# Kernel tuning notes

Hardware: AMD Instinct MI355X
Metric: run time of the kernel (lower is better)

Reference implementation:

```python
import jax, jax.numpy as jnp
import numpy as np

B, T, V, H, NH, NLVL = 64, 2048, 256, 64, 4, 2
HD = H // NH  # 16
EPS = 1e-5


def setup_inputs() -> dict:
    key = jax.random.key(0)
    ks = jax.random.split(key, 16)
    s = 0.05
    return {
        "x": jax.random.randint(ks[0], (B, T), 0, V),
        "emb": jax.random.normal(ks[1], (V, H), dtype=jnp.float32) * s,
        # LSTM params, PyTorch gate order i, f, g, o stacked along dim 0
        "w_ih": jax.random.normal(ks[2], (4 * H, H), dtype=jnp.float32) * s,
        "w_hh": jax.random.normal(ks[3], (4 * H, H), dtype=jnp.float32) * s,
        "b_ih": jax.random.normal(ks[4], (4 * H,), dtype=jnp.float32) * s,
        "b_hh": jax.random.normal(ks[5], (4 * H,), dtype=jnp.float32) * s,
        # two MHA levels, packed qkv in_proj like nn.MultiheadAttention
        "wqkv": jax.random.normal(ks[6], (NLVL, 3 * H, H), dtype=jnp.float32) * s,
        "bqkv": jax.random.normal(ks[7], (NLVL, 3 * H), dtype=jnp.float32) * s,
        "wo": jax.random.normal(ks[8], (NLVL, H, H), dtype=jnp.float32) * s,
        "bo": jax.random.normal(ks[9], (NLVL, H), dtype=jnp.float32) * s,
        "ln_g": jnp.ones((H,), dtype=jnp.float32),
        "ln_b": jnp.zeros((H,), dtype=jnp.float32),
        "fc_w": jax.random.normal(ks[10], (V, H), dtype=jnp.float32) * s,
        "fc_b": jax.random.normal(ks[11], (V,), dtype=jnp.float32) * s,
    }


def _lstm(x, w_ih, w_hh, b_ih, b_hh):
    # x: (B, T, H) -> (B, T, H); single layer, PyTorch gate order i,f,g,o
    b = x.shape[0]
    h0 = jnp.zeros((b, H), x.dtype)
    c0 = jnp.zeros((b, H), x.dtype)

    def step(carry, xt):
        h, c = carry
        g = xt @ w_ih.T + b_ih + h @ w_hh.T + b_hh  # (B, 4H)
        i, f, gg, o = jnp.split(g, 4, axis=-1)
        c = jax.nn.sigmoid(f) * c + jax.nn.sigmoid(i) * jnp.tanh(gg)
        h = jax.nn.sigmoid(o) * jnpp_tanh(c) if False else jax.nn.sigmoid(o) * jnp.tanh(c)
        return (h, c), h

    _, hs = jax.lax.scan(step, (h0, c0), jnp.swapaxes(x, 0, 1))  # (T, B, H)
    return jnp.swapaxes(hs, 0, 1)


def _mha(x, wqkv, bqkv, wo, bo):
    # Faithful to nn.MultiheadAttention with batch_first=False:
    # x: (L, N, E) where here L = batch dim of lstm_out, N = seq dim.
    L, N, E = x.shape
    qkv = x @ wqkv.T + bqkv  # (L, N, 3E)
    q, k, v = jnp.split(qkv, 3, axis=-1)
    q = q.reshape(L, N, NH, HD)
    k = k.reshape(L, N, NH, HD)
    v = v.reshape(L, N, NH, HD)
    scale = jnp.asarray(1.0 / np.sqrt(HD), x.dtype)
    att = jax.nn.softmax(jnp.einsum('lnhd,mnhd->nhlm', q, k) * scale, axis=-1)
    o = jnp.einsum('nhlm,mnhd->lnhd', att, v).reshape(L, N, E)
    return o @ wo.T + bo


def reference(x, emb, w_ih, w_hh, b_ih, b_hh, wqkv, bqkv, wo, bo, ln_g, ln_b, fc_w, fc_b):
    h = emb[x]  # (B, T, H)
    h = _lstm(h, w_ih, w_hh, b_ih, b_hh)  # (B, T, H)
    for l in range(NLVL):
        h = _mha(h, wqkv[l], bqkv[l], wo[l], bo[l])
    mu = jnp.mean(h, axis=-1, keepdims=True)
    var = jnp.mean(jnp.square(h - mu), axis=-1, keepdims=True)  # biased, like torch LN
    hn = (h - mu) * jax.lax.rsqrt(var + EPS) * ln_g + ln_b
    return hn @ fc_w.T + fc_b  # (B, T, V)
```

## Files before the change

### kernel.cpp

```cpp
#include <hip/hip_runtime.h>

enum { TT = 2048, HH = 64, BB = 64, GG = 256, VV = 256 };

static __device__ __forceinline__ void bar_lds(){
  asm volatile("s_waitcnt lgkmcnt(0)\n\ts_barrier" ::: "memory");
}

__global__ __launch_bounds__(256) void k_embw(const float* __restrict__ emb,
                                              const float* __restrict__ w_ih,
                                              const float* __restrict__ b_ih,
                                              const float* __restrict__ b_hh,
                                              float* __restrict__ embW){
  int v = blockIdx.x, g = threadIdx.x;
  __shared__ float e[HH];
  if (g < HH) e[g] = emb[v*HH + g];
  bar_lds();
  float acc = b_ih[g] + b_hh[g];
  const float* wr = w_ih + g*HH;
#pragma unroll
  for (int k = 0; k < HH; k += 4){
    float4 w4 = *(const float4*)(wr + k);
    acc = fmaf(e[k],   w4.x, acc); acc = fmaf(e[k+1], w4.y, acc);
    acc = fmaf(e[k+2], w4.z, acc); acc = fmaf(e[k+3], w4.w, acc);
  }
  embW[v*GG + g] = acc;
}

__global__ __launch_bounds__(256) void k_lstm(const int* __restrict__ x,
                                              const float* __restrict__ embW,
                                              const float* __restrict__ w_hh,
                                              float* __restrict__ hout){
  int b = blockIdx.x, g = threadIdx.x;
  __shared__ float hsh[HH];
  __shared__ float gsh[GG];
  float w[HH];
  {
    const float* wr = w_hh + g*HH;
#pragma unroll
    for (int k = 0; k < HH; k += 4)
      *(float4*)&w[k] = *(const float4*)(wr + k);
  }
  if (g < HH) hsh[g] = 0.f;
  float c = 0.f;
  const int* xb = x + b*TT;
  int i0 = xb[0];
  float gx = embW[i0*GG + g];
  int i1 = xb[1];
  const bool istanh = ((g >> 6) == 2);
  float* houtb = hout + (size_t)b*TT*HH;
  bar_lds();
#pragma unroll 2
  for (int t = 0; t < TT; t++){
    float gxn = embW[i1*GG + g];
    int inx = xb[(t + 2 < TT) ? (t + 2) : (TT - 1)];
    float a0 = 0.f, a1 = 0.f, a2 = 0.f, a3 = 0.f;
#pragma unroll
    for (int k = 0; k < 16; k += 4){
      float4 h0 = *(const float4*)&hsh[k];
      float4 h1 = *(const float4*)&hsh[16 + k];
      float4 h2 = *(const float4*)&hsh[32 + k];
      float4 h3 = *(const float4*)&hsh[48 + k];
      a0 = fmaf(w[k],      h0.x, a0); a0 = fmaf(w[k+1],    h0.y, a0);
      a0 = fmaf(w[k+2],    h0.z, a0); a0 = fmaf(w[k+3],    h0.w, a0);
      a1 = fmaf(w[16+k],   h1.x, a1); a1 = fmaf(w[16+k+1], h1.y, a1);
      a1 = fmaf(w[16+k+2], h1.z, a1); a1 = fmaf(w[16+k+3], h1.w, a1);
      a2 = fmaf(w[32+k],   h2.x, a2); a2 = fmaf(w[32+k+1], h2.y, a2);
      a2 = fmaf(w[32+k+2], h2.z, a2); a2 = fmaf(w[32+k+3], h2.w, a2);
      a3 = fmaf(w[48+k],   h3.x, a3); a3 = fmaf(w[48+k+1], h3.y, a3);
      a3 = fmaf(w[48+k+2], h3.z, a3); a3 = fmaf(w[48+k+3], h3.w, a3);
    }
    float acc = ((a0 + a1) + (a2 + a3)) + gx;
    float val;
    if (istanh) val = 1.f - 2.f/(__expf(2.f*acc) + 1.f);
    else        val = 1.f/(1.f + __expf(-acc));
    gsh[g] = val;
    bar_lds();
    if (g < HH){
      float i_ = gsh[g], f_ = gsh[HH+g], gg = gsh[128+g], o_ = gsh[192+g];
      c = fmaf(f_, c, i_*gg);
      float th = 1.f - 2.f/(__expf(2.f*c) + 1.f);
      float hv = o_*th;
      hsh[g] = hv;
      houtb[(size_t)t*HH + g] = hv;
    }
    bar_lds();
    gx = gxn; i1 = inx;
  }
}

__global__ __launch_bounds__(256) void k_mha(const float* __restrict__ hin,
                                             const float* __restrict__ wqkv,
                                             const float* __restrict__ bqkv,
                                             const float* __restrict__ wo,
                                             const float* __restrict__ bo,
                                             float* __restrict__ hout){
  int t = blockIdx.x, tid = threadIdx.x;
  __shared__ float xta[BB][HH];
  __shared__ float qkvs[BB][192];

  float wq[HH]; float bq = 0.f;
  if (tid < 192){
#pragma unroll
    for (int k = 0; k < HH; k += 4)
      *(float4*)&wq[k] = *(const float4*)(wqkv + tid*HH + k);
    bq = bqkv[tid];
  }
  {
    int r = tid >> 2, q = tid & 3;
    const float* p = hin + (size_t)(r*TT + t)*HH + q*16;
#pragma unroll
    for (int j = 0; j < 16; j += 4)
      *(float4*)&xta[r][q*16 + j] = *(const float4*)(p + j);
  }
  bar_lds();
  if (tid < 192){
#pragma unroll 4
    for (int b = 0; b < BB; b++){
      float acc = bq;
#pragma unroll
      for (int k = 0; k < HH; k += 4){
        float4 xv = *(const float4*)&xta[b][k];
        acc = fmaf(wq[k],   xv.x, acc); acc = fmaf(wq[k+1], xv.y, acc);
        acc = fmaf(wq[k+2], xv.z, acc); acc = fmaf(wq[k+3], xv.w, acc);
      }
      qkvs[b][tid] = acc;
    }
  }
  bar_lds();
  {
    int hd = tid >> 6, l = tid & 63;
    int qo = hd*16, ko = 64 + hd*16, vo = 128 + hd*16;
    float4 q0 = *(const float4*)&qkvs[l][qo];
    float4 q1 = *(const float4*)&qkvs[l][qo+4];
    float4 q2 = *(const float4*)&qkvs[l][qo+8];
    float4 q3 = *(const float4*)&qkvs[l][qo+12];
    float S[BB];
#pragma unroll
    for (int m = 0; m < BB; m++){
      float4 k0 = *(const float4*)&qkvs[m][ko];
      float4 k1 = *(const float4*)&qkvs[m][ko+4];
      float4 k2 = *(const float4*)&qkvs[m][ko+8];
      float4 k3 = *(const float4*)&qkvs[m][ko+12];
      float d;
      d = q0.x*k0.x;         d = fmaf(q0.y,k0.y,d); d = fmaf(q0.z,k0.z,d); d = fmaf(q0.w,k0.w,d);
      d = fmaf(q1.x,k1.x,d); d = fmaf(q1.y,k1.y,d); d = fmaf(q1.z,k1.z,d); d = fmaf(q1.w,k1.w,d);
      d = fmaf(q2.x,k2.x,d); d = fmaf(q2.y,k2.y,d); d = fmaf(q2.z,k2.z,d); d = fmaf(q2.w,k2.w,d);
      d = fmaf(q3.x,k3.x,d); d = fmaf(q3.y,k3.y,d); d = fmaf(q3.z,k3.z,d); d = fmaf(q3.w,k3.w,d);
      S[m] = 0.25f*d;
    }
    float mx = S[0];
#pragma unroll
    for (int m = 1; m < BB; m++) mx = fmaxf(mx, S[m]);
    float sum = 0.f;
#pragma unroll
    for (int m = 0; m < BB; m++){ S[m] = __expf(S[m] - mx); sum += S[m]; }
    float inv = 1.f/sum;
    float4 a0 = make_float4(0,0,0,0), a1 = a0, a2 = a0, a3 = a0;
#pragma unroll
    for (int m = 0; m < BB; m++){
      float s = S[m];
      float4 v0 = *(const float4*)&qkvs[m][vo];
      float4 v1 = *(const float4*)&qkvs[m][vo+4];
      float4 v2 = *(const float4*)&qkvs[m][vo+8];
      float4 v3 = *(const float4*)&qkvs[m][vo+12];
      a0.x = fmaf(s,v0.x,a0.x); a0.y = fmaf(s,v0.y,a0.y); a0.z = fmaf(s,v0.z,a0.z); a0.w = fmaf(s,v0.w,a0.w);
      a1.x = fmaf(s,v1.x,a1.x); a1.y = fmaf(s,v1.y,a1.y); a1.z = fmaf(s,v1.z,a1.z); a1.w = fmaf(s,v1.w,a1.w);
      a2.x = fmaf(s,v2.x,a2.x); a2.y = fmaf(s,v2.y,a2.y); a2.z = fmaf(s,v2.z,a2.z); a2.w = fmaf(s,v2.w,a2.w);
      a3.x = fmaf(s,v3.x,a3.x); a3.y = fmaf(s,v3.y,a3.y); a3.z = fmaf(s,v3.z,a3.z); a3.w = fmaf(s,v3.w,a3.w);
    }
    a0.x*=inv; a0.y*=inv; a0.z*=inv; a0.w*=inv;
    a1.x*=inv; a1.y*=inv; a1.z*=inv; a1.w*=inv;
    a2.x*=inv; a2.y*=inv; a2.z*=inv; a2.w*=inv;
    a3.x*=inv; a3.y*=inv; a3.z*=inv; a3.w*=inv;
    bar_lds();
    *(float4*)&xta[l][qo]    = a0;
    *(float4*)&xta[l][qo+4]  = a1;
    *(float4*)&xta[l][qo+8]  = a2;
    *(float4*)&xta[l][qo+12] = a3;
  }
  bar_lds();
  {
    int c = tid & 63, wg = tid >> 6;
    float wor[HH];
#pragma unroll
    for (int k = 0; k < HH; k += 4)
      *(float4*)&wor[k] = *(const float4*)(wo + c*HH + k);
    float bo4 = bo[c];
#pragma unroll 2
    for (int j = 0; j < 16; j++){
      int b = wg*16 + j;
      float acc = bo4;
#pragma unroll
      for (int k = 0; k < HH; k += 4){
        float4 xv = *(const float4*)&xta[b][k];
        acc = fmaf(wor[k],   xv.x, acc); acc = fmaf(wor[k+1], xv.y, acc);
        acc = fmaf(wor[k+2], xv.z, acc); acc = fmaf(wor[k+3], xv.w, acc);
      }
      hout[(size_t)(b*TT + t)*HH + c] = acc;
    }
  }
}

__global__ __launch_bounds__(256) void k_fc(const float* __restrict__ hin,
                                            const float* __restrict__ ln_g,
                                            const float* __restrict__ ln_b,
                                            const float* __restrict__ fc_w,
                                            const float* __restrict__ fc_b,
                                            float* __restrict__ out){
  int tid = threadIdx.x;
  __shared__ float tile[64][68];
  __shared__ float ps[64][4];
  __shared__ float pq[64][4];
  __shared__ float mu[64], rs[64];
  float w[HH];
  float wsum = 0.f, bias2 = fc_b[tid];
#pragma unroll
  for (int k = 0; k < HH; k += 4){
    float4 wv = *(const float4*)(fc_w + tid*HH + k);
    float4 gv = *(const float4*)(ln_g + k);
    float4 bv = *(const float4*)(ln_b + k);
    bias2 = fmaf(bv.x, wv.x, bias2); bias2 = fmaf(bv.y, wv.y, bias2);
    bias2 = fmaf(bv.z, wv.z, bias2); bias2 = fmaf(bv.w, wv.w, bias2);
    w[k]   = gv.x*wv.x; w[k+1] = gv.y*wv.y;
    w[k+2] = gv.z*wv.z; w[k+3] = gv.w*wv.w;
    wsum += w[k] + w[k+1] + w[k+2] + w[k+3];
  }
  int r = tid >> 2, q = tid & 3;
  for (int ti = 0; ti < 4; ti++){
    int rowbase = blockIdx.x*256 + ti*64;
    const float* p = hin + (size_t)(rowbase + r)*HH + q*16;
    float xv[16];
#pragma unroll
    for (int j = 0; j < 16; j += 4)
      *(float4*)&xv[j] = *(const float4*)(p + j);
    float s1 = 0.f, s2 = 0.f;
#pragma unroll
    for (int j = 0; j < 16; j++){ s1 += xv[j]; s2 = fmaf(xv[j], xv[j], s2); }
#pragma unroll
    for (int j = 0; j < 16; j += 4)
      *(float4*)&tile[r][q*16 + j] = *(const float4*)&xv[j];
    ps[r][q] = s1; pq[r][q] = s2;
    bar_lds();
    if (tid < 64){
      float4 a  = *(const float4*)&ps[tid][0];
      float4 b4 = *(const float4*)&pq[tid][0];
      float m = (a.x + a.y + a.z + a.w) * (1.f/64.f);
      float v = (b4.x + b4.y + b4.z + b4.w) * (1.f/64.f) - m*m;
      mu[tid] = m;
      rs[tid] = rsqrtf(v + 1e-5f);
    }
    bar_lds();
#pragma unroll 2
    for (int rr = 0; rr < 64; rr++){
      float acc = 0.f;
#pragma unroll
      for (int k = 0; k < HH; k += 4){
        float4 x4 = *(const float4*)&tile[rr][k];
        acc = fmaf(w[k],   x4.x, acc); acc = fmaf(w[k+1], x4.y, acc);
        acc = fmaf(w[k+2], x4.z, acc); acc = fmaf(w[k+3], x4.w, acc);
      }
      float o = rs[rr]*(acc - mu[rr]*wsum) + bias2;
      out[(size_t)(rowbase + rr)*VV + tid] = o;
    }
    bar_lds();
  }
}

extern "C" void kernel_launch(void* const* d_in, const int* in_sizes, int n_in,
                              void* d_out, int out_size, void* d_ws, size_t ws_size,
                              hipStream_t stream){
  (void)in_sizes; (void)n_in; (void)out_size; (void)ws_size;
  const int*   x    = (const int*)d_in[0];
  const float* emb  = (const float*)d_in[1];
  const float* w_ih = (const float*)d_in[2];
  const float* w_hh = (const float*)d_in[3];
  const float* b_ih = (const float*)d_in[4];
  const float* b_hh = (const float*)d_in[5];
  const float* wqkv = (const float*)d_in[6];
  const float* bqkv = (const float*)d_in[7];
  const float* wo   = (const float*)d_in[8];
  const float* bo   = (const float*)d_in[9];
  const float* ln_g = (const float*)d_in[10];
  const float* ln_b = (const float*)d_in[11];
  const float* fc_w = (const float*)d_in[12];
  const float* fc_b = (const float*)d_in[13];

  char* ws = (char*)d_ws;
  float* embW = (float*)ws;
  float* bufA = (float*)(ws + (1<<20));
  float* bufB = bufA + (size_t)BB*TT*HH;

  k_embw<<<VV,  256, 0, stream>>>(emb, w_ih, b_ih, b_hh, embW);
  k_lstm<<<BB,  256, 0, stream>>>(x, embW, w_hh, bufA);
  k_mha <<<TT,  256, 0, stream>>>(bufA, wqkv,          bqkv,       wo,          bo,      bufB);
  k_mha <<<TT,  256, 0, stream>>>(bufB, wqkv + 192*64, bqkv + 192, wo + 64*64,  bo + 64, bufA);
  k_fc  <<<512, 256, 0, stream>>>(bufA, ln_g, ln_b, fc_w, fc_b, (float*)d_out);
}
```

Before: 1.760 ms.

## Exchange LSTM gates via wave shuffles and double-buffer hidden state

Threads are remapped so that each wavefront holds the i, f, g and o gate rows for the same 16 hidden elements. Gate values are then combined with cross-lane shuffles instead of being written to and read back from shared memory. The hidden state is double-buffered in LDS, which removes one of the two block barriers in every one of the 2048 serial timesteps. The tanh gate is rewritten as a scaled sigmoid so all lanes take the same branch-free path. In exchange, three quarters of the lanes compute a cell update that is thrown away.

```diff
diff --git a/kernel.cpp b/kernel.cpp
--- a/kernel.cpp
+++ b/kernel.cpp
@@ -30,36 +30,40 @@
                                               const float* __restrict__ embW,
                                               const float* __restrict__ w_hh,
                                               float* __restrict__ hout){
-  int b = blockIdx.x, g = threadIdx.x;
-  __shared__ float hsh[HH];
-  __shared__ float gsh[GG];
+  int b = blockIdx.x, tid = threadIdx.x;
+  int wq = tid >> 6, l = tid & 63;
+  int grp = l >> 4, sub = l & 15;
+  int elem = wq*16 + sub;
+  int row  = grp*64 + elem;
+  __shared__ __align__(16) float hbuf[2][HH];
   float w[HH];
   {
-    const float* wr = w_hh + g*HH;
+    const float* wr = w_hh + row*HH;
 #pragma unroll
     for (int k = 0; k < HH; k += 4)
       *(float4*)&w[k] = *(const float4*)(wr + k);
   }
-  if (g < HH) hsh[g] = 0.f;
+  if (tid < HH) hbuf[0][tid] = 0.f;
   float c = 0.f;
   const int* xb = x + b*TT;
   int i0 = xb[0];
-  float gx = embW[i0*GG + g];
+  float gx = embW[i0*GG + row];
   int i1 = xb[1];
-  const bool istanh = ((g >> 6) == 2);
+  const bool g2 = (grp == 2);
   float* houtb = hout + (size_t)b*TT*HH;
   bar_lds();
 #pragma unroll 2
   for (int t = 0; t < TT; t++){
-    float gxn = embW[i1*GG + g];
+    float gxn = embW[i1*GG + row];
     int inx = xb[(t + 2 < TT) ? (t + 2) : (TT - 1)];
+    const float* hb = hbuf[t & 1];
     float a0 = 0.f, a1 = 0.f, a2 = 0.f, a3 = 0.f;
 #pragma unroll
     for (int k = 0; k < 16; k += 4){
-      float4 h0 = *(const float4*)&hsh[k];
-      float4 h1 = *(const float4*)&hsh[16 + k];
-      float4 h2 = *(const float4*)&hsh[32 + k];
-      float4 h3 = *(const float4*)&hsh[48 + k];
+      float4 h0 = *(const float4*)&hb[k];
+      float4 h1 = *(const float4*)&hb[16 + k];
+      float4 h2 = *(const float4*)&hb[32 + k];
+      float4 h3 = *(const float4*)&hb[48 + k];
       a0 = fmaf(w[k],      h0.x, a0); a0 = fmaf(w[k+1],    h0.y, a0);
       a0 = fmaf(w[k+2],    h0.z, a0); a0 = fmaf(w[k+3],    h0.w, a0);
       a1 = fmaf(w[16+k],   h1.x, a1); a1 = fmaf(w[16+k+1], h1.y, a1);
@@ -70,18 +74,20 @@
       a3 = fmaf(w[48+k+2], h3.z, a3); a3 = fmaf(w[48+k+3], h3.w, a3);
     }
     float acc = ((a0 + a1) + (a2 + a3)) + gx;
-    float val;
-    if (istanh) val = 1.f - 2.f/(__expf(2.f*acc) + 1.f);
-    else        val = 1.f/(1.f + __expf(-acc));
-    gsh[g] = val;
-    bar_lds();
-    if (g < HH){
-      float i_ = gsh[g], f_ = gsh[HH+g], gg = gsh[128+g], o_ = gsh[192+g];
-      c = fmaf(f_, c, i_*gg);
-      float th = 1.f - 2.f/(__expf(2.f*c) + 1.f);
-      float hv = o_*th;
-      hsh[g] = hv;
-      houtb[(size_t)t*HH + g] = hv;
+    float arg = g2 ? (2.f*acc) : acc;
+    float s   = 1.f/(1.f + __expf(-arg));
+    float val = g2 ? fmaf(2.f, s, -1.f) : s;
+    float vi = val;
+    float vf = __shfl_xor(val, 16);
+    float vg = __shfl_xor(val, 32);
+    float vo = __shfl_xor(val, 48);
+    c = fmaf(vf, c, vi*vg);
+    float e2 = __expf(2.f*c);
+    float th = 1.f - 2.f/(e2 + 1.f);
+    float h  = vo*th;
+    if (l < 16){
+      hbuf[(t + 1) & 1][elem] = h;
+      houtb[(size_t)t*HH + elem] = h;
     }
     bar_lds();
     gx = gxn; i1 = inx;
```

Result: slower. 1.847 ms (+4.9%).

## Run LSTM recurrence in a single wavefront, one hidden unit per lane

Applied to the files above, without the earlier changes.

The LSTM kernel drops from 256 threads per batch row to one 64-lane wavefront. Each lane keeps all four gate weight rows in registers and computes its own i, f, g, o gates, so the intermediate gate exchange through LDS and both per-step block barriers go away. In exchange each lane does four times the FMA work per step, and holding 256 weight values per lane creates heavy register pressure and a possible spill risk. Correctness relies on in-order LDS access within a single wavefront rather than on an explicit barrier.

```diff
diff --git a/kernel.cpp b/kernel.cpp
--- a/kernel.cpp
+++ b/kernel.cpp
@@ -26,65 +26,66 @@
   embW[v*GG + g] = acc;
 }
 
-__global__ __launch_bounds__(256) void k_lstm(const int* __restrict__ x,
-                                              const float* __restrict__ embW,
-                                              const float* __restrict__ w_hh,
-                                              float* __restrict__ hout){
-  int b = blockIdx.x, g = threadIdx.x;
-  __shared__ float hsh[HH];
-  __shared__ float gsh[GG];
-  float w[HH];
-  {
-    const float* wr = w_hh + g*HH;
-#pragma unroll
-    for (int k = 0; k < HH; k += 4)
-      *(float4*)&w[k] = *(const float4*)(wr + k);
-  }
-  if (g < HH) hsh[g] = 0.f;
+__global__ __launch_bounds__(64) void k_lstm(const int* __restrict__ x,
+                                             const float* __restrict__ embW,
+                                             const float* __restrict__ w_hh,
+                                             float* __restrict__ hout){
+  int b = blockIdx.x, l = threadIdx.x;
+  __shared__ __align__(16) float hsh[HH];
+  float4 wi[16], wf[16], wg[16], wo4[16];
+  {
+    const float* ri = w_hh + (l      )*HH;
+    const float* rf = w_hh + (l +  64)*HH;
+    const float* rg = w_hh + (l + 128)*HH;
+    const float* ro = w_hh + (l + 192)*HH;
+#pragma unroll
+    for (int k = 0; k < 16; k++){
+      wi[k]  = *(const float4*)(ri + 4*k);
+      wf[k]  = *(const float4*)(rf + 4*k);
+      wg[k]  = *(const float4*)(rg + 4*k);
+      wo4[k] = *(const float4*)(ro + 4*k);
+    }
+  }
+  hsh[l] = 0.f;
   float c = 0.f;
   const int* xb = x + b*TT;
   int i0 = xb[0];
-  float gx = embW[i0*GG + g];
+  float gi = embW[i0*GG +       l];
+  float gf = embW[i0*GG +  64 + l];
+  float gg = embW[i0*GG + 128 + l];
+  float go = embW[i0*GG + 192 + l];
   int i1 = xb[1];
-  const bool istanh = ((g >> 6) == 2);
   float* houtb = hout + (size_t)b*TT*HH;
-  bar_lds();
-#pragma unroll 2
+  const float4* hp = (const float4*)hsh;
   for (int t = 0; t < TT; t++){
-    float gxn = embW[i1*GG + g];
+    float gi_n = embW[i1*GG +       l];
+    float gf_n = embW[i1*GG +  64 + l];
+    float gg_n = embW[i1*GG + 128 + l];
+    float go_n = embW[i1*GG + 192 + l];
     int inx = xb[(t + 2 < TT) ? (t + 2) : (TT - 1)];
-    float a0 = 0.f, a1 = 0.f, a2 = 0.f, a3 = 0.f;
-#pragma unroll
-    for (int k = 0; k < 16; k += 4){
-      float4 h0 = *(const float4*)&hsh[k];
-      float4 h1 = *(const float4*)&hsh[16 + k];
-      float4 h2 = *(const float4*)&hsh[32 + k];
-      float4 h3 = *(const float4*)&hsh[48 + k];
-      a0 = fmaf(w[k],      h0.x, a0); a0 = fmaf(w[k+1],    h0.y, a0);
-      a0 = fmaf(w[k+2],    h0.z, a0); a0 = fmaf(w[k+3],    h0.w, a0);
-      a1 = fmaf(w[16+k],   h1.x, a1); a1 = fmaf(w[16+k+1], h1.y, a1);
-      a1 = fmaf(w[16+k+2], h1.z, a1); a1 = fmaf(w[16+k+3], h1.w, a1);
-      a2 = fmaf(w[32+k],   h2.x, a2); a2 = fmaf(w[32+k+1], h2.y, a2);
-      a2 = fmaf(w[32+k+2], h2.z, a2); a2 = fmaf(w[32+k+3], h2.w, a2);
-      a3 = fmaf(w[48+k],   h3.x, a3); a3 = fmaf(w[48+k+1], h3.y, a3);
-      a3 = fmaf(w[48+k+2], h3.z, a3); a3 = fmaf(w[48+k+3], h3.w, a3);
-    }
-    float acc = ((a0 + a1) + (a2 + a3)) + gx;
-    float val;
-    if (istanh) val = 1.f - 2.f/(__expf(2.f*acc) + 1.f);
-    else        val = 1.f/(1.f + __expf(-acc));
-    gsh[g] = val;
-    bar_lds();
-    if (g < HH){
-      float i_ = gsh[g], f_ = gsh[HH+g], gg = gsh[128+g], o_ = gsh[192+g];
-      c = fmaf(f_, c, i_*gg);
-      float th = 1.f - 2.f/(__expf(2.f*c) + 1.f);
-      float hv = o_*th;
-      hsh[g] = hv;
-      houtb[(size_t)t*HH + g] = hv;
-    }
-    bar_lds();
-    gx = gxn; i1 = inx;
+    float ai = gi, af = gf, ag = gg, ao = go;
+#pragma unroll
+    for (int k = 0; k < 16; k++){
+      float4 hv = hp[k];
+      ai = fmaf(wi[k].x,  hv.x, ai); ai = fmaf(wi[k].y,  hv.y, ai);
+      ai = fmaf(wi[k].z,  hv.z, ai); ai = fmaf(wi[k].w,  hv.w, ai);
+      af = fmaf(wf[k].x,  hv.x, af); af = fmaf(wf[k].y,  hv.y, af);
+      af = fmaf(wf[k].z,  hv.z, af); af = fmaf(wf[k].w,  hv.w, af);
+      ag = fmaf(wg[k].x,  hv.x, ag); ag = fmaf(wg[k].y,  hv.y, ag);
+      ag = fmaf(wg[k].z,  hv.z, ag); ag = fmaf(wg[k].w,  hv.w, ag);
+      ao = fmaf(wo4[k].x, hv.x, ao); ao = fmaf(wo4[k].y, hv.y, ao);
+      ao = fmaf(wo4[k].z, hv.z, ao); ao = fmaf(wo4[k].w, hv.w, ao);
+    }
+    float vi = 1.f/(1.f + __expf(-ai));
+    float vf = 1.f/(1.f + __expf(-af));
+    float vg = 1.f - 2.f/(__expf(2.f*ag) + 1.f);
+    float vo = 1.f/(1.f + __expf(-ao));
+    c = fmaf(vf, c, vi*vg);
+    float th = 1.f - 2.f/(__expf(2.f*c) + 1.f);
+    float h  = vo*th;
+    hsh[l] = h;
+    houtb[(size_t)t*HH + l] = h;
+    gi = gi_n; gf = gf_n; gg = gg_n; go = go_n; i1 = inx;
   }
 }
 
@@ -291,7 +292,7 @@
   float* bufB = bufA + (size_t)BB*TT*HH;
 
   k_embw<<<VV,  256, 0, stream>>>(emb, w_ih, b_ih, b_hh, embW);
-  k_lstm<<<BB,  256, 0, stream>>>(x, embW, w_hh, bufA);
+  k_lstm<<<BB,   64, 0, stream>>>(x, embW, w_hh, bufA);
   k_mha <<<TT,  256, 0, stream>>>(bufA, wqkv,          bqkv,       wo,          bo,      bufB);
   k_mha <<<TT,  256, 0, stream>>>(bufB, wqkv + 192*64, bqkv + 192, wo + 64*64,  bo + 64, bufA);
   k_fc  <<<512, 256, 0, stream>>>(bufA, ln_g, ln_b, fc_w, fc_b, (float*)d_out);
```

Result: slower. 3.078 ms (+74.9%).
